# Performance work log

Measured on AMD Instinct MI355X. Metric: run time of the kernel, lower is better.

The kernel has to match this reference:

```python
import jax, jax.numpy as jnp
import numpy as np

B, I, C, J, D, H, W = 16, 32, 8, 10, 16, 6, 6
NUM_ROUTING = 3
EPS = 1e-07


def setup_inputs() -> dict:
    key = jax.random.key(0)
    u_hat = jax.random.normal(key, (B, I, C, J, D, H, W), dtype=jnp.float32)
    # torch module fills bias with 0.1, shape (out_capsules, out_channels, 1, 1)
    bias = jnp.full((J, D, 1, 1), 0.1, dtype=jnp.float32)
    return {"u_hat": u_hat, "bias": bias, "num_routing": NUM_ROUTING}


def _squash(s):
    # Faithful to the source: L1 norm over ALL non-batch dims (not per-capsule L2).
    n1 = jnp.sum(jnp.abs(s), axis=(1, 2, 3, 4), keepdims=True)  # [B,1,1,1,1]
    n1_sq = n1 * n1
    return (n1_sq / (1.0 + n1_sq)) * (s / (n1 + EPS))


def reference(u_hat, bias, num_routing):
    # u_hat: [B,I,C,J,D,H,W]; bias: [J,D,1,1]
    b_ij = jnp.zeros((I, J), dtype=u_hat.dtype)
    v_j = None
    for _ in range(num_routing):
        c_ij = jax.nn.softmax(b_ij, axis=1)  # [I,J]
        # s_j[b,j,d,h,w] = sum_{i,c} c[i,j] * u_hat[b,i,c,j,d,h,w]  (c broadcast over in_channels)
        s_j = jnp.einsum('ij,bicjdhw->bjdhw', c_ij, u_hat) + bias
        v_j = _squash(s_j)  # [B,J,D,H,W]
        # agreement[i,j] = sum over b,c,d,h,w of u_hat * v_j (broadcast over i,c)
        agreement = jnp.einsum('bicjdhw,bjdhw->ij', u_hat, v_j)
        b_ij = b_ij + jax.lax.stop_gradient(agreement)  # torch uses .data (detached)
    return v_j
```

## Files before the change

kernel.cpp:

```cpp
#include <hip/hip_runtime.h>


#define NB   16
#define NI   32
#define NC   8
#define NJ   10
#define ND   16
#define NHW  36
#define NDHW 576
#define NBJ  (NB * NJ)
#define NTOT (NB * NJ * NDHW)
#define EPSV 1e-7f
#define TPB  576
#define GP_ITER (NJ * NI * NB)
#define GP_J    (NI * NB)
#define GP_I    (NB)
#define N1_ITER (NB * NJ)
#define N1_B    (NJ)

static __device__ __forceinline__ double wave_sum(double v) {
    #pragma unroll
    for (int off = 32; off > 0; off >>= 1) v += __shfl_down(v, off);
    return v;
}

static __device__ __forceinline__ void n1_reduce(float sv, double* slot,
                                                 double* nred ) {
    int tid = threadIdx.x;
    double a = wave_sum((double)fabsf(sv));
    if ((tid & 63) == 0) nred[tid >> 6] = a;
    __syncthreads();
    if (tid == 0) {
        double t = nred[0];
        #pragma unroll
        for (int w = 1; w < 9; ++w) t += nred[w];
        *slot = t;
    }
}

static __device__ __forceinline__ void g_reduce_t(const float* Uv, float sv,
                                                  double* gbase,
                                                  double (*gred)[32] ) {
    int tid = threadIdx.x, w = tid >> 6, lane = tid & 63;
    #pragma unroll
    for (int i = 0; i < NI; ++i) {
        double p = wave_sum((double)Uv[i] * (double)sv);
        if (lane == 0) gred[w][i] = p;
    }
    __syncthreads();
    if (tid < NI) {
        double t = gred[0][tid];
        #pragma unroll
        for (int w2 = 1; w2 < 9; ++w2) t += gred[w2][tid];
        gbase[tid * GP_I] = t;
    }
}

__global__ __launch_bounds__(TPB) void a1_kernel(
    const float4* __restrict__ uh4, const float* __restrict__ bias,
    float4* __restrict__ U2f4, double* __restrict__ n1p, double* __restrict__ Gp)
{
    __shared__ float4  Utile4[NI * 144];
    __shared__ double  nred[9];
    __shared__ double  gred[9][32];

    const int blk = blockIdx.x;
    const int b = blk / NJ, j = blk - b * NJ;
    const int tid = threadIdx.x;

    #pragma unroll
    for (int g = 0; g < 8; ++g) {
        int lin = g * TPB + tid;
        int i  = lin / 144, f4 = lin - i * 144;
        const float4* p = uh4 + ((size_t)(b * NI + i) * NC) * 1440 + j * 144 + f4;
        float4 acc = make_float4(0.f, 0.f, 0.f, 0.f);
        #pragma unroll
        for (int c = 0; c < NC; ++c) {
            float4 v = p[(size_t)c * 1440];
            acc.x += v.x; acc.y += v.y; acc.z += v.z; acc.w += v.w;
        }
        Utile4[lin] = acc;
        U2f4[(size_t)blk * 4608 + lin] = acc;
    }
    __syncthreads();

    const float* Utile = (const float*)Utile4;
    const float cw = 1.0f / 10.0f;
    float Uv[NI];
    float sv = bias[j * ND + tid / NHW];
    #pragma unroll
    for (int i = 0; i < NI; ++i) {
        Uv[i] = Utile[i * NDHW + tid];
        sv += cw * Uv[i];
    }

    n1_reduce(sv, &n1p[b * N1_B + j], nred);
    g_reduce_t(Uv, sv, Gp + j * GP_J + b, gred);
}

__global__ __launch_bounds__(TPB) void ab1_kernel(
    const float* __restrict__ U2, const float* __restrict__ bias,
    double* __restrict__ n1p, double* __restrict__ Gp)
{
    __shared__ double sc_sh[NB];
    __shared__ float  bij_sh[NI * NJ];
    __shared__ float  c_sh[NI];
    __shared__ double nred[9];
    __shared__ double gred[9][32];

    const int blk = blockIdx.x;
    const int b = blk / NJ, j = blk - b * NJ;
    const int tid = threadIdx.x;

    if (tid < NB) {
        const double* np = n1p + tid * N1_B;
        double n1 = 0.0;
        #pragma unroll
        for (int jj = 0; jj < NJ; ++jj) n1 += np[jj];
        double nsq = n1 * n1;
        sc_sh[tid] = (nsq / (1.0 + nsq)) / (n1 + (double)EPSV);
    }
    __syncthreads();

    if (tid < NI * NJ) {
        int i = tid / NJ, jj = tid - i * NJ;
        const double* g = Gp + jj * GP_J + i * GP_I;
        double a = 0.0;
        #pragma unroll
        for (int bb = 0; bb < NB; ++bb) a += sc_sh[bb] * g[bb];
        bij_sh[tid] = (float)a;
    }
    __syncthreads();

    if (tid < NI) {
        float m = -1e30f;
        #pragma unroll
        for (int jj = 0; jj < NJ; ++jj) m = fmaxf(m, bij_sh[tid * NJ + jj]);
        float sum = 0.f;
        #pragma unroll
        for (int jj = 0; jj < NJ; ++jj) sum += expf(bij_sh[tid * NJ + jj] - m);
        c_sh[tid] = expf(bij_sh[tid * NJ + j] - m) / sum;
    }
    __syncthreads();

    const float* u2b = U2 + (size_t)b * (NJ * NI * NDHW) + j * (NI * NDHW) + tid;
    float Uv[NI];
    float sv = bias[j * ND + tid / NHW];
    #pragma unroll
    for (int i = 0; i < NI; ++i) {
        Uv[i] = u2b[i * NDHW];
        sv += c_sh[i] * Uv[i];
    }

    n1_reduce(sv, &n1p[N1_ITER + b * N1_B + j], nred);
    g_reduce_t(Uv, sv, Gp + GP_ITER + j * GP_J + b, gred);
}

__global__ __launch_bounds__(TPB) void final_kernel(
    const float* __restrict__ U2, const float* __restrict__ bias,
    const double* __restrict__ n1p, const double* __restrict__ Gp,
    float* __restrict__ out)
{
    __shared__ double sc_sh[2][NB];
    __shared__ float  bij_sh[NI * NJ];
    __shared__ float  c_sh[NI * NJ];
    __shared__ double nred[9];
    __shared__ double n1_sh;

    const int blk = blockIdx.x;
    const int b = blk & (NB - 1), j = blk >> 4;
    const int tid = threadIdx.x;

    if (tid < 2 * NB) {
        int rr = tid >> 4, bb = tid & 15;
        const double* np = n1p + rr * N1_ITER + bb * N1_B;
        double n1 = 0.0;
        #pragma unroll
        for (int jj = 0; jj < NJ; ++jj) n1 += np[jj];
        double nsq = n1 * n1;
        sc_sh[rr][bb] = (nsq / (1.0 + nsq)) / (n1 + (double)EPSV);
    }
    __syncthreads();

    if (tid < NI * NJ) {
        int i = tid / NJ, jj = tid - i * NJ;
        double a = 0.0;
        for (int rr = 0; rr < 2; ++rr) {
            const double* g = Gp + rr * GP_ITER + jj * GP_J + i * GP_I;
            #pragma unroll
            for (int bb = 0; bb < NB; ++bb) a += sc_sh[rr][bb] * g[bb];
        }
        bij_sh[tid] = (float)a;
    }
    __syncthreads();

    if (tid < NI * NJ) {
        int i = tid / NJ;
        float m = -1e30f;
        #pragma unroll
        for (int j2 = 0; j2 < NJ; ++j2) m = fmaxf(m, bij_sh[i * NJ + j2]);
        float sum = 0.f;
        #pragma unroll
        for (int j2 = 0; j2 < NJ; ++j2) sum += expf(bij_sh[i * NJ + j2] - m);
        c_sh[tid] = expf(bij_sh[tid] - m) / sum;
    }
    __syncthreads();

    const float* ub = U2 + (size_t)b * (NJ * NI * NDHW) + tid;
    const int drow = tid / NHW;
    double t = 0.0;
    float sv_out = 0.f;
    #pragma unroll 1
    for (int jj = 0; jj < NJ; ++jj) {
        const float* up = ub + jj * (NI * NDHW);
        float sv = bias[jj * ND + drow];
        #pragma unroll
        for (int i = 0; i < NI; ++i) sv += c_sh[i * NJ + jj] * up[i * NDHW];
        t += (double)fabsf(sv);
        if (jj == j) sv_out = sv;
    }

    double a = wave_sum(t);
    if ((tid & 63) == 0) nred[tid >> 6] = a;
    __syncthreads();
    if (tid == 0) {
        double n1 = nred[0];
        #pragma unroll
        for (int w = 1; w < 9; ++w) n1 += nred[w];
        n1_sh = n1;
    }
    __syncthreads();

    float n1f = (float)n1_sh;
    float nsq = n1f * n1f;
    out[(size_t)(b * NJ + j) * NDHW + tid] =
        (nsq / (1.f + nsq)) * (sv_out / (n1f + EPSV));
}

extern "C" void kernel_launch(void* const* d_in, const int* in_sizes, int n_in,
                              void* d_out, int out_size, void* d_ws, size_t ws_size,
                              hipStream_t stream)
{
    const float* u_hat = (const float*)d_in[0];
    const float* bias  = (const float*)d_in[1];
    float* out = (float*)d_out;

    float*  U2  = (float*)d_ws;
    double* n1p = (double*)(U2 + (size_t)NB * NJ * NI * NDHW);
    double* Gp  = n1p + 2 * N1_ITER;

    a1_kernel<<<NBJ, TPB, 0, stream>>>(
        (const float4*)u_hat, bias, (float4*)U2, n1p, Gp);
    ab1_kernel<<<NBJ, TPB, 0, stream>>>(U2, bias, n1p, Gp);
    final_kernel<<<NBJ, TPB, 0, stream>>>(U2, bias, n1p, Gp, out);
}
```

Baseline: 182.0 us.

## Split channel-sum into dedicated streaming kernel and relayout U2 as [b,i,j,dhw]

```diff
diff --git a/kernel.cpp b/kernel.cpp
--- a/kernel.cpp
+++ b/kernel.cpp
@@ -12,6 +12,8 @@
 #define NTOT (NB * NJ * NDHW)
 #define EPSV 1e-7f
 #define TPB  576
+#define UWB  256
+#define U2_I 5760
 #define GP_ITER (NJ * NI * NB)
 #define GP_J    (NI * NB)
 #define GP_I    (NB)
@@ -56,41 +58,61 @@
     }
 }
 
-__global__ __launch_bounds__(TPB) void a1_kernel(
-    const float4* __restrict__ uh4, const float* __restrict__ bias,
-    float4* __restrict__ U2f4, double* __restrict__ n1p, double* __restrict__ Gp)
-{
-    __shared__ float4  Utile4[NI * 144];
-    __shared__ double  nred[9];
-    __shared__ double  gred[9][32];
+__global__ __launch_bounds__(UWB) void uw_kernel(
+    const float4* __restrict__ uh4, float4* __restrict__ U2f4)
+{
+    const int blk = blockIdx.x;
+    const int tid = threadIdx.x;
+    const float4* in  = uh4 + (size_t)blk * (NC * 1440);
+    float4*       out = U2f4 + (size_t)blk * 1440;
+
+    float4 acc[6];
+    #pragma unroll
+    for (int r = 0; r < 6; ++r) acc[r] = make_float4(0.f, 0.f, 0.f, 0.f);
+
+    #pragma unroll
+    for (int c = 0; c < NC; ++c) {
+        const float4* pc = in + c * 1440;
+        float4 v[6];
+        #pragma unroll
+        for (int r = 0; r < 6; ++r) {
+            int o = r * UWB + tid;
+            if (o < 1440) v[r] = pc[o];
+        }
+        #pragma unroll
+        for (int r = 0; r < 6; ++r) {
+            int o = r * UWB + tid;
+            if (o < 1440) {
+                acc[r].x += v[r].x; acc[r].y += v[r].y;
+                acc[r].z += v[r].z; acc[r].w += v[r].w;
+            }
+        }
+    }
+    #pragma unroll
+    for (int r = 0; r < 6; ++r) {
+        int o = r * UWB + tid;
+        if (o < 1440) out[o] = acc[r];
+    }
+}
+
+__global__ __launch_bounds__(TPB) void it0_kernel(
+    const float* __restrict__ U2, const float* __restrict__ bias,
+    double* __restrict__ n1p, double* __restrict__ Gp)
+{
+    __shared__ double nred[9];
+    __shared__ double gred[9][32];
 
     const int blk = blockIdx.x;
     const int b = blk / NJ, j = blk - b * NJ;
     const int tid = threadIdx.x;
 
-    #pragma unroll
-    for (int g = 0; g < 8; ++g) {
-        int lin = g * TPB + tid;
-        int i  = lin / 144, f4 = lin - i * 144;
-        const float4* p = uh4 + ((size_t)(b * NI + i) * NC) * 1440 + j * 144 + f4;
-        float4 acc = make_float4(0.f, 0.f, 0.f, 0.f);
-        #pragma unroll
-        for (int c = 0; c < NC; ++c) {
-            float4 v = p[(size_t)c * 1440];
-            acc.x += v.x; acc.y += v.y; acc.z += v.z; acc.w += v.w;
-        }
-        Utile4[lin] = acc;
-        U2f4[(size_t)blk * 4608 + lin] = acc;
-    }
-    __syncthreads();
-
-    const float* Utile = (const float*)Utile4;
+    const float* u2b = U2 + (size_t)(b * NI) * U2_I + j * NDHW + tid;
     const float cw = 1.0f / 10.0f;
     float Uv[NI];
     float sv = bias[j * ND + tid / NHW];
     #pragma unroll
     for (int i = 0; i < NI; ++i) {
-        Uv[i] = Utile[i * NDHW + tid];
+        Uv[i] = u2b[(size_t)i * U2_I];
         sv += cw * Uv[i];
     }
 
@@ -143,12 +165,12 @@
     }
     __syncthreads();
 
-    const float* u2b = U2 + (size_t)b * (NJ * NI * NDHW) + j * (NI * NDHW) + tid;
+    const float* u2b = U2 + (size_t)(b * NI) * U2_I + j * NDHW + tid;
     float Uv[NI];
     float sv = bias[j * ND + tid / NHW];
     #pragma unroll
     for (int i = 0; i < NI; ++i) {
-        Uv[i] = u2b[i * NDHW];
+        Uv[i] = u2b[(size_t)i * U2_I];
         sv += c_sh[i] * Uv[i];
     }
 
@@ -206,16 +228,16 @@
     }
     __syncthreads();
 
-    const float* ub = U2 + (size_t)b * (NJ * NI * NDHW) + tid;
+    const float* ub = U2 + (size_t)(b * NI) * U2_I + tid;
     const int drow = tid / NHW;
     double t = 0.0;
     float sv_out = 0.f;
     #pragma unroll 1
     for (int jj = 0; jj < NJ; ++jj) {
-        const float* up = ub + jj * (NI * NDHW);
+        const float* up = ub + jj * NDHW;
         float sv = bias[jj * ND + drow];
         #pragma unroll
-        for (int i = 0; i < NI; ++i) sv += c_sh[i * NJ + jj] * up[i * NDHW];
+        for (int i = 0; i < NI; ++i) sv += c_sh[i * NJ + jj] * up[(size_t)i * U2_I];
         t += (double)fabsf(sv);
         if (jj == j) sv_out = sv;
     }
@@ -249,8 +271,9 @@
     double* n1p = (double*)(U2 + (size_t)NB * NJ * NI * NDHW);
     double* Gp  = n1p + 2 * N1_ITER;
 
-    a1_kernel<<<NBJ, TPB, 0, stream>>>(
-        (const float4*)u_hat, bias, (float4*)U2, n1p, Gp);
+    uw_kernel<<<NB * NI, UWB, 0, stream>>>(
+        (const float4*)u_hat, (float4*)U2);
+    it0_kernel<<<NBJ, TPB, 0, stream>>>(U2, bias, n1p, Gp);
     ab1_kernel<<<NBJ, TPB, 0, stream>>>(U2, bias, n1p, Gp);
     final_kernel<<<NBJ, TPB, 0, stream>>>(U2, bias, n1p, Gp, out);
 }
```

After: 184.3 us. No clear change (+1.3%).
